# Optimization experiments

Measured on AMD Instinct MI355X. Metric: run time of the kernel, lower is better.

The kernel has to match this reference:

```python
import jax, jax.numpy as jnp
import numpy as np

N = 10000       # nodes
E = 160000      # edges (avg degree 16)
F_IN = 5        # node feature dim
ED = 2          # edge feature dim


def _tconv(x, src, dst, ea, Wq, bq, Wk, bk, Wv, bv, We, Ws, bs, heads, C, concat):
    """PyG TransformerConv (eval mode, root_weight=True, beta=False)."""
    n = x.shape[0]
    q = (x @ Wq + bq).reshape(n, heads, C)
    k = (x @ Wk + bk).reshape(n, heads, C)
    v = (x @ Wv + bv).reshape(n, heads, C)
    e = (ea @ We).reshape(ea.shape[0], heads, C)          # edge embedding, added to key and value
    kj = k[src] + e                                        # [E,H,C] gather source keys
    vj = v[src] + e                                        # [E,H,C] gather source values
    logits = jnp.einsum('ehc,ehc->eh', q[dst], kj) / jnp.sqrt(jnp.asarray(C, x.dtype))
    m = jax.ops.segment_max(logits, dst, num_segments=n)   # stable segment softmax over in-edges
    p = jnp.exp(logits - m[dst])
    s = jax.ops.segment_sum(p, dst, num_segments=n)
    alpha = p / s[dst]                                     # [E,H]
    out = jax.ops.segment_sum(alpha[..., None] * vj, dst, num_segments=n)  # [N,H,C]
    out = out.reshape(n, heads * C) if concat else jnp.mean(out, axis=1)
    return out + x @ Ws + bs                               # root/skip connection


def setup_inputs() -> dict:
    key = jax.random.key(0)
    keys = iter(jax.random.split(key, 64))
    def p(shape):
        return jax.random.normal(next(keys), shape, jnp.float32) * 0.05
    inp = {}
    inp['x'] = jax.random.normal(next(keys), (N, F_IN), jnp.float32)
    inp['edge_src'] = jax.random.randint(next(keys), (E,), 0, N)
    inp['edge_dst'] = jax.random.randint(next(keys), (E,), 0, N)
    inp['edge_attr'] = jax.random.normal(next(keys), (E, ED), jnp.float32)
    # (in_dim, heads, out_channels, concat) for the 3 TransformerConv layers
    layers = [(F_IN, 4, 128, True), (512, 4, 128, True), (512, 1, 64, False)]
    for i, (fin, h, c, concat) in enumerate(layers, 1):
        hc = h * c
        sk = hc if concat else c
        inp[f'Wq{i}'] = p((fin, hc)); inp[f'bq{i}'] = p((hc,))
        inp[f'Wk{i}'] = p((fin, hc)); inp[f'bk{i}'] = p((hc,))
        inp[f'Wv{i}'] = p((fin, hc)); inp[f'bv{i}'] = p((hc,))
        inp[f'We{i}'] = p((ED, hc))   # lin_edge has no bias in PyG
        inp[f'Ws{i}'] = p((fin, sk)); inp[f'bs{i}'] = p((sk,))
    return inp


def reference(x, edge_src, edge_dst, edge_attr,
              Wq1, bq1, Wk1, bk1, Wv1, bv1, We1, Ws1, bs1,
              Wq2, bq2, Wk2, bk2, Wv2, bv2, We2, Ws2, bs2,
              Wq3, bq3, Wk3, bk3, Wv3, bv3, We3, Ws3, bs3):
    h = jax.nn.relu(_tconv(x, edge_src, edge_dst, edge_attr,
                           Wq1, bq1, Wk1, bk1, Wv1, bv1, We1, Ws1, bs1, 4, 128, True))
    h = jax.nn.relu(_tconv(h, edge_src, edge_dst, edge_attr,
                           Wq2, bq2, Wk2, bk2, Wv2, bv2, We2, Ws2, bs2, 4, 128, True))
    return _tconv(h, edge_src, edge_dst, edge_attr,
                  Wq3, bq3, Wk3, bk3, Wv3, bv3, We3, Ws3, bs3, 1, 64, False)
```

## Files before the change

kernel.cpp:

```cpp
#include <hip/hip_runtime.h>

typedef unsigned short u16;
typedef __attribute__((ext_vector_type(8))) short bf16x8;
typedef __attribute__((ext_vector_type(4))) float f32x4;

__device__ __forceinline__ float bf2f(u16 s) {
    return __uint_as_float(((unsigned)s) << 16);
}
__device__ __forceinline__ u16 f2bf(float f) {
    unsigned u = __float_as_uint(f);
    u += 0x7fff + ((u >> 16) & 1);
    return (u16)(u >> 16);
}
__device__ __forceinline__ void unpack8(bf16x8 x, float* f) {
#pragma unroll
    for (int j = 0; j < 8; ++j) f[j] = bf2f((u16)x[j]);
}

__device__ __forceinline__ void gload16(const u16* g, u16* l) {
    __builtin_amdgcn_global_load_lds(
        (const __attribute__((address_space(1))) unsigned*)g,
        (__attribute__((address_space(3))) unsigned*)l, 16, 0, 0);
}

__device__ __forceinline__ float dot8(bf16x8 a, bf16x8 b, float c) {
#if __has_builtin(__builtin_amdgcn_fdot2_f32_bf16)
    typedef __attribute__((ext_vector_type(2))) __bf16 bf16x2;
    union U { bf16x8 v; bf16x2 p[4]; };
    U ua, ub; ua.v = a; ub.v = b;
#pragma unroll
    for (int i = 0; i < 4; ++i)
        c = __builtin_amdgcn_fdot2_f32_bf16(ua.p[i], ub.p[i], c, false);
    return c;
#else
    float fa[8], fb[8];
    unpack8(a, fa); unpack8(b, fb);
#pragma unroll
    for (int j = 0; j < 8; ++j) c = fmaf(fa[j], fb[j], c);
    return c;
#endif
}

struct Ptr8 { const float* p[8]; };
struct PrepArgs { const float* w[8]; const float* b[8]; };

__global__ __launch_bounds__(256)
void prep_weights(PrepArgs a, u16* __restrict__ Wt2, u16* __restrict__ Wt3,
                  float* __restrict__ b2, float* __restrict__ b3) {
    int z = blockIdx.z;
    if (z == 8) {
        if (blockIdx.y != 0 || blockIdx.x >= 9) return;
        int j = blockIdx.x * 256 + threadIdx.x;
        if (j < 2048) b2[j] = a.b[j >> 9][j & 511];
        else if (j < 2304) { int jj = j - 2048; b3[jj] = a.b[4 + (jj >> 6)][jj & 63]; }
        return;
    }
    const float* in;
    u16* out;
    int Nw;
    if (z < 4) { in = a.w[z]; out = Wt2 + (size_t)z * 512 * 512; Nw = 512; }
    else {
        if (blockIdx.y >= 2) return;
        in = a.w[z]; out = Wt3 + (size_t)(z - 4) * 64 * 512; Nw = 64;
    }
    __shared__ float t[32][33];
    int kb = blockIdx.x * 32, nb = blockIdx.y * 32;
    int tx = threadIdx.x & 31, ty = threadIdx.x >> 5;
#pragma unroll
    for (int r = ty; r < 32; r += 8)
        if (nb + tx < Nw)
            t[r][tx] = in[(size_t)(kb + r) * Nw + nb + tx];
    __syncthreads();
#pragma unroll
    for (int r = ty; r < 32; r += 8)
        if (nb + r < Nw)
            out[(size_t)(nb + r) * 512 + kb + tx] = f2bf(t[tx][r]);
}

__global__ __launch_bounds__(256)
void gemm_l1(const float* __restrict__ X, Ptr8 wb, u16* __restrict__ OUT, int N) {
    int wsel = threadIdx.x >> 6;
    int jj = (threadIdx.x & 63) * 8;
    const float* W = wb.p[wsel];
    const float* b = wb.p[4 + wsel];
    float w[5][8], bs[8];
#pragma unroll
    for (int i = 0; i < 5; ++i)
#pragma unroll
        for (int j = 0; j < 8; ++j) w[i][j] = W[(size_t)i * 512 + jj + j];
#pragma unroll
    for (int j = 0; j < 8; ++j) bs[j] = b[jj + j];
    int n0 = blockIdx.x * 8;
    int nend = (N - n0 < 8) ? (N - n0) : 8;
    for (int i = 0; i < nend; ++i) {
        int n = n0 + i;
        float xr[5];
#pragma unroll
        for (int k = 0; k < 5; ++k) xr[k] = X[(size_t)n * 5 + k];
        float acc[8];
#pragma unroll
        for (int j = 0; j < 8; ++j) acc[j] = bs[j];
#pragma unroll
        for (int k = 0; k < 5; ++k)
#pragma unroll
            for (int j = 0; j < 8; ++j) acc[j] = fmaf(xr[k], w[k][j], acc[j]);
        bf16x8 o;
#pragma unroll
        for (int j = 0; j < 8; ++j) o[j] = (short)f2bf(acc[j]);
        *(bf16x8*)(OUT + (size_t)n * 2048 + wsel * 512 + jj) = o;
    }
}

template <int TN>
__global__ __launch_bounds__(256)
void gemm_bf16(const u16* __restrict__ A, const u16* __restrict__ Bt,
               const float* __restrict__ bias, u16* __restrict__ C,
               int M, int Ncols, int K) {
    constexpr int TM = 128, BK = 64;
    constexpr int MFR = (TN == 128) ? 4 : 2;
    constexpr int NFR = 4;
    constexpr int ACH = TM * BK / (256 * 8);
    constexpr int BCH = TN * BK / (256 * 8);

    __shared__ u16 As[TM * BK];
    __shared__ u16 Bs[TN * BK];

    int tid = threadIdx.x;
    int lane = tid & 63;
    int w = tid >> 6;
    int rowbase = blockIdx.x * TM;
    int colbase = blockIdx.y * TN;
    int mwave = (TN == 128) ? (w >> 1) * 64 : w * 32;
    int nwave = (TN == 128) ? (w & 1) * 64 : 0;

    f32x4 acc[MFR][NFR] = {};

    int arow[ACH], asl[ACH];
#pragma unroll
    for (int c = 0; c < ACH; ++c) {
        int idx = c * 256 + tid;
        arow[c] = idx >> 3;
        asl[c] = (idx & 7) ^ (arow[c] & 7);
    }

    for (int k0 = 0; k0 < K; k0 += BK) {
#pragma unroll
        for (int c = 0; c < ACH; ++c) {
            int idx = c * 256 + tid;
            int gr = rowbase + arow[c]; if (gr > M - 1) gr = M - 1;
            gload16(A + (size_t)gr * K + k0 + asl[c] * 8, &As[idx * 8]);
        }
#pragma unroll
        for (int c = 0; c < BCH; ++c) {
            int idx = c * 256 + tid;
            int row = idx >> 3, sl = (idx & 7) ^ (row & 7);
            gload16(Bt + (size_t)(colbase + row) * K + k0 + sl * 8, &Bs[idx * 8]);
        }
        __syncthreads();
#pragma unroll
        for (int kh = 0; kh < 2; ++kh) {
            bf16x8 af[MFR], bfr[NFR];
            int ks = (lane >> 4) + kh * 4;
#pragma unroll
            for (int mi = 0; mi < MFR; ++mi) {
                int r = mwave + mi * 16 + (lane & 15);
                af[mi] = *(const bf16x8*)&As[r * BK + ((ks ^ (r & 7)) * 8)];
            }
#pragma unroll
            for (int ni = 0; ni < NFR; ++ni) {
                int r = nwave + ni * 16 + (lane & 15);
                bfr[ni] = *(const bf16x8*)&Bs[r * BK + ((ks ^ (r & 7)) * 8)];
            }
#pragma unroll
            for (int mi = 0; mi < MFR; ++mi)
#pragma unroll
                for (int ni = 0; ni < NFR; ++ni)
                    acc[mi][ni] = __builtin_amdgcn_mfma_f32_16x16x32_bf16(
                        af[mi], bfr[ni], acc[mi][ni], 0, 0, 0);
        }
        __syncthreads();
    }
#pragma unroll
    for (int mi = 0; mi < MFR; ++mi) {
        int r0 = rowbase + mwave + mi * 16 + (lane >> 4) * 4;
#pragma unroll
        for (int ni = 0; ni < NFR; ++ni) {
            int col = colbase + nwave + ni * 16 + (lane & 15);
            float bv = bias[col];
#pragma unroll
            for (int r = 0; r < 4; ++r) {
                int row = r0 + r;
                if (row < M)
                    C[(size_t)row * Ncols + col] = f2bf(acc[mi][ni][r] + bv);
            }
        }
    }
}

__global__ __launch_bounds__(256)
void histo_dst(const int* __restrict__ dst, int* __restrict__ deg, int E) {
    int i = blockIdx.x * 256 + threadIdx.x;
    if (i < E) atomicAdd(&deg[dst[i]], 1);
}

__global__ __launch_bounds__(1024)
void scan_deg(const int* __restrict__ deg, int* __restrict__ off,
              int* __restrict__ cur, int N) {
    __shared__ int part[1024];
    int t = threadIdx.x;
    int per = (N + 1023) / 1024;
    int base = t * per;
    int s = 0;
    for (int i = 0; i < per; ++i)
        if (base + i < N) s += deg[base + i];
    part[t] = s;
    __syncthreads();
    for (int d = 1; d < 1024; d <<= 1) {
        int v = (t >= d) ? part[t - d] : 0;
        __syncthreads();
        part[t] += v;
        __syncthreads();
    }
    int excl = (t > 0) ? part[t - 1] : 0;
    for (int i = 0; i < per; ++i) {
        int n = base + i;
        if (n < N) {
            off[n] = excl;
            cur[n] = excl;
            excl += deg[n];
        }
    }
    if (t == 1023) off[N] = part[1023];
}

__global__ __launch_bounds__(256)
void scatter_edges(const int* __restrict__ src, const int* __restrict__ dst,
                   const float* __restrict__ EA, int* __restrict__ cur,
                   int* __restrict__ csrc, float2* __restrict__ caxy, int E) {
    int i = blockIdx.x * 256 + threadIdx.x;
    if (i < E) {
        int p = atomicAdd(&cur[dst[i]], 1);
        csrc[p] = src[i];
        caxy[p] = *(const float2*)(EA + 2 * (size_t)i);
    }
}

template <bool RELU>
__global__ __launch_bounds__(256)
void node_attn4(const u16* __restrict__ QKVS, const int* __restrict__ csrc,
                const float2* __restrict__ caxy, const float* __restrict__ We,
                const int* __restrict__ off, u16* __restrict__ OUT,
                int N, float scale) {
    constexpr int SR = 2048, koff = 512, voff = 1024, skoff = 1536;
    constexpr int HC = 512, C = 128, LPG = 16;
    int n = blockIdx.x;
    int w = threadIdx.x >> 6;
    int lane = threadIdx.x & 63;
    int g = lane / LPG;
    int li = lane % LPG;
    int cc = g * C + li * 8;

    const float sc2 = scale * 1.44269504f;
    const u16* nrow = QKVS + (size_t)n * SR;
    bf16x8 q8 = *(const bf16x8*)(nrow + cc);
    float qf[8];
    unpack8(q8, qf);

    float qw0 = 0.f, qw1 = 0.f;
    {
        f32x4 wa = *(const f32x4*)(We + cc), wb = *(const f32x4*)(We + cc + 4);
        f32x4 wc = *(const f32x4*)(We + HC + cc), wd = *(const f32x4*)(We + HC + cc + 4);
#pragma unroll
        for (int j = 0; j < 4; ++j) {
            qw0 = fmaf(qf[j], wa[j], qw0); qw0 = fmaf(qf[4 + j], wb[j], qw0);
            qw1 = fmaf(qf[j], wc[j], qw1); qw1 = fmaf(qf[4 + j], wd[j], qw1);
        }
    }
#pragma unroll
    for (int d = 1; d < LPG; d <<= 1) {
        qw0 += __shfl_xor(qw0, d);
        qw1 += __shfl_xor(qw1, d);
    }
    qw0 *= sc2; qw1 *= sc2;

    int base = off[n];
    int deg = off[n + 1] - base;
    int pdeg = deg < 64 ? deg : 64;
    int ps = 0; float pax = 0.f, pay = 0.f;
    int el = w + 4 * lane;
    if (lane < 16 && el < pdeg) {
        ps = csrc[base + el];
        float2 a = caxy[base + el];
        pax = a.x; pay = a.y;
    }
    int wdeg = (pdeg > w) ? ((pdeg - w + 3) >> 2) : 0;

    float s = 0.f, A0 = 0.f, A1 = 0.f;
    float acc[8] = {};
    const u16* Kp = QKVS + koff;
    const u16* Vp = QKVS + voff;

    auto process = [&](float ax, float ay, bf16x8 k8, bf16x8 v8) {
        float qk = dot8(q8, k8, 0.f);
#pragma unroll
        for (int d = 1; d < LPG; d <<= 1) qk += __shfl_xor(qk, d);
        float lg2 = fmaf(qk, sc2, fmaf(ax, qw0, ay * qw1));
        lg2 = fminf(lg2, 80.f);
        float p = exp2f(lg2);
        s += p;
        A0 = fmaf(p, ax, A0);
        A1 = fmaf(p, ay, A1);
        float vf[8];
        unpack8(v8, vf);
#pragma unroll
        for (int j = 0; j < 8; ++j) acc[j] = fmaf(p, vf[j], acc[j]);
    };

    auto ldp = [&](int t, bf16x8& k8, bf16x8& v8) {
        int tt = t < wdeg ? t : 0;
        int s0 = __shfl(ps, tt);
        k8 = *(const bf16x8*)(Kp + (size_t)s0 * SR + cc);
        v8 = *(const bf16x8*)(Vp + (size_t)s0 * SR + cc);
    };
    if (wdeg > 0) {
        bf16x8 ka0, va0, ka1, va1, kb0, vb0, kb1, vb1;
        ldp(0, ka0, va0); ldp(1, ka1, va1);
        ldp(2, kb0, vb0); ldp(3, kb1, vb1);
        int t = 0;
        for (; t + 2 < wdeg; t += 4) {
            float ax, ay;
            ax = __shfl(pax, t); ay = __shfl(pay, t);
            process(ax, ay, ka0, va0);
            ax = __shfl(pax, t + 1); ay = __shfl(pay, t + 1);
            process(ax, ay, ka1, va1);
            ldp(t + 4, ka0, va0); ldp(t + 5, ka1, va1);
            ax = __shfl(pax, t + 2); ay = __shfl(pay, t + 2);
            process(ax, ay, kb0, vb0);
            if (t + 3 < wdeg) {
                ax = __shfl(pax, t + 3); ay = __shfl(pay, t + 3);
                process(ax, ay, kb1, vb1);
            }
            ldp(t + 6, kb0, vb0); ldp(t + 7, kb1, vb1);
        }
        if (t < wdeg) {
            float ax = __shfl(pax, t), ay = __shfl(pay, t);
            process(ax, ay, ka0, va0);
        }
        if (t + 1 < wdeg) {
            float ax = __shfl(pax, t + 1), ay = __shfl(pay, t + 1);
            process(ax, ay, ka1, va1);
        }
    }
    for (int idx = 64 + w; idx < deg; idx += 4) {
        int s0 = csrc[base + idx];
        float2 a = caxy[base + idx];
        bf16x8 k0 = *(const bf16x8*)(Kp + (size_t)s0 * SR + cc);
        bf16x8 v0 = *(const bf16x8*)(Vp + (size_t)s0 * SR + cc);
        process(a.x, a.y, k0, v0);
    }

    __shared__ float sm[3][64][13];
    if (w > 0) {
        float* d = sm[w - 1][lane];
        d[0] = s; d[1] = A0; d[2] = A1;
#pragma unroll
        for (int j = 0; j < 8; ++j) d[3 + j] = acc[j];
    }
    __syncthreads();
    if (w == 0) {
#pragma unroll
        for (int wv = 0; wv < 3; ++wv) {
            const float* d = sm[wv][lane];
            s += d[0]; A0 += d[1]; A1 += d[2];
#pragma unroll
            for (int j = 0; j < 8; ++j) acc[j] += d[3 + j];
        }
        float inv = (s > 0.f) ? 1.f / s : 0.f;
        float sk[8];
        unpack8(*(const bf16x8*)(nrow + skoff + cc), sk);
        f32x4 wa = *(const f32x4*)(We + cc), wb = *(const f32x4*)(We + cc + 4);
        f32x4 wc = *(const f32x4*)(We + HC + cc), wd = *(const f32x4*)(We + HC + cc + 4);
        float w0[8] = {wa[0], wa[1], wa[2], wa[3], wb[0], wb[1], wb[2], wb[3]};
        float w1[8] = {wc[0], wc[1], wc[2], wc[3], wd[0], wd[1], wd[2], wd[3]};
        bf16x8 ov;
#pragma unroll
        for (int j = 0; j < 8; ++j) {
            float agg = (acc[j] + A0 * w0[j] + A1 * w1[j]) * inv;
            float o = agg + sk[j];
            if (RELU) o = fmaxf(o, 0.f);
            ov[j] = (short)f2bf(o);
        }
        *(bf16x8*)(OUT + (size_t)n * 512 + cc) = ov;
    }
}

template <int H, int C, int LPG, bool RELU>
__global__ __launch_bounds__(256)
void node_attn(const u16* __restrict__ QKVS, int SR, int koff, int voff,
               int skoff, const int* __restrict__ csrc,
               const float2* __restrict__ caxy, const float* __restrict__ We,
               const int* __restrict__ off, float* __restrict__ OUT,
               int OST, int N, float scale) {
    constexpr int HC = H * C;
    constexpr int NG = 64 / LPG;
    int n = blockIdx.x * 4 + (threadIdx.x >> 6);
    if (n >= N) return;
    int lane = threadIdx.x & 63;
    int g = lane / LPG;
    int li = lane % LPG;
    int cc = li * 8;

    const float sc2 = scale * 1.44269504f;
    const u16* nrow = QKVS + (size_t)n * SR;
    bf16x8 q8 = *(const bf16x8*)(nrow + cc);
    float qf[8];
    unpack8(q8, qf);

    float qw0 = 0.f, qw1 = 0.f;
    {
        f32x4 wa = *(const f32x4*)(We + cc), wb = *(const f32x4*)(We + cc + 4);
        f32x4 wc = *(const f32x4*)(We + HC + cc), wd = *(const f32x4*)(We + HC + cc + 4);
#pragma unroll
        for (int j = 0; j < 4; ++j) {
            qw0 = fmaf(qf[j], wa[j], qw0); qw0 = fmaf(qf[4 + j], wb[j], qw0);
            qw1 = fmaf(qf[j], wc[j], qw1); qw1 = fmaf(qf[4 + j], wd[j], qw1);
        }
    }
#pragma unroll
    for (int d = 1; d < LPG; d <<= 1) {
        qw0 += __shfl_xor(qw0, d);
        qw1 += __shfl_xor(qw1, d);
    }
    qw0 *= sc2; qw1 *= sc2;

    int base = off[n];
    int deg = off[n + 1] - base;
    int pdeg = deg < 64 ? deg : 64;
    int ps = 0; float pax = 0.f, pay = 0.f;
    if (lane < pdeg) {
        ps = csrc[base + lane];
        float2 a = caxy[base + lane];
        pax = a.x; pay = a.y;
    }

    float s = 0.f, A0 = 0.f, A1 = 0.f;
    float acc[8] = {};
    const u16* Kp = QKVS + koff;
    const u16* Vp = QKVS + voff;

    auto process = [&](float ax, float ay, bf16x8 k8, bf16x8 v8) {
        float qk = dot8(q8, k8, 0.f);
#pragma unroll
        for (int d = 1; d < LPG; d <<= 1) qk += __shfl_xor(qk, d);
        float lg2 = fmaf(qk, sc2, fmaf(ax, qw0, ay * qw1));
        lg2 = fminf(lg2, 80.f);
        float p = exp2f(lg2);
        s += p;
        A0 = fmaf(p, ax, A0);
        A1 = fmaf(p, ay, A1);
        float vf[8];
        unpack8(v8, vf);
#pragma unroll
        for (int j = 0; j < 8; ++j) acc[j] = fmaf(p, vf[j], acc[j]);
    };

    int trips = (pdeg + NG - 1) / NG;
    for (int k = 0; k < trips; ++k) {
        int idx = g + NG * k;
        bool valid = idx < pdeg;
        int sidx = valid ? idx : (pdeg - 1);
        int s0 = __shfl(ps, sidx);
        float ax0 = __shfl(pax, sidx), ay0 = __shfl(pay, sidx);
        bf16x8 k0 = *(const bf16x8*)(Kp + (size_t)s0 * SR + cc);
        bf16x8 v0 = *(const bf16x8*)(Vp + (size_t)s0 * SR + cc);
        if (valid) process(ax0, ay0, k0, v0);
    }
    int otr = (deg > 64) ? (deg - 64 + NG - 1) / NG : 0;
    for (int k = 0; k < otr; ++k) {
        int idx = 64 + NG * k + g;
        bool valid = idx < deg;
        int ii = valid ? idx : (deg - 1);
        int s0 = csrc[base + ii];
        float2 a = caxy[base + ii];
        bf16x8 k0 = *(const bf16x8*)(Kp + (size_t)s0 * SR + cc);
        bf16x8 v0 = *(const bf16x8*)(Vp + (size_t)s0 * SR + cc);
        if (valid) process(a.x, a.y, k0, v0);
    }
#pragma unroll
    for (int d = LPG; d < 64; d <<= 1) {
        s += __shfl_xor(s, d);
        A0 += __shfl_xor(A0, d);
        A1 += __shfl_xor(A1, d);
#pragma unroll
        for (int j = 0; j < 8; ++j) acc[j] += __shfl_xor(acc[j], d);
    }

    if (g == 0) {
        float inv = (s > 0.f) ? 1.f / s : 0.f;
        float sk[8];
        unpack8(*(const bf16x8*)(nrow + skoff + cc), sk);
        f32x4 wa = *(const f32x4*)(We + cc), wb = *(const f32x4*)(We + cc + 4);
        f32x4 wc = *(const f32x4*)(We + HC + cc), wd = *(const f32x4*)(We + HC + cc + 4);
        float w0[8] = {wa[0], wa[1], wa[2], wa[3], wb[0], wb[1], wb[2], wb[3]};
        float w1[8] = {wc[0], wc[1], wc[2], wc[3], wd[0], wd[1], wd[2], wd[3]};
        float o[8];
#pragma unroll
        for (int j = 0; j < 8; ++j) {
            float agg = (acc[j] + A0 * w0[j] + A1 * w1[j]) * inv;
            o[j] = agg + sk[j];
            if (RELU) o[j] = fmaxf(o[j], 0.f);
        }
        f32x4 oa = {o[0], o[1], o[2], o[3]}, ob = {o[4], o[5], o[6], o[7]};
        *(f32x4*)(OUT + (size_t)n * OST + cc) = oa;
        *(f32x4*)(OUT + (size_t)n * OST + cc + 4) = ob;
    }
}

extern "C" void kernel_launch(void* const* d_in, const int* in_sizes, int n_in,
                              void* d_out, int out_size, void* d_ws, size_t ws_size,
                              hipStream_t stream) {
    const float* x  = (const float*)d_in[0];
    const int* esrc = (const int*)d_in[1];
    const int* edst = (const int*)d_in[2];
    const float* ea = (const float*)d_in[3];
    const int N = in_sizes[0] / 5;
    const int E = in_sizes[1];
    auto in = [&](int i) { return (const float*)d_in[i]; };

    char* p = (char*)d_ws;
    auto alloc = [&](size_t b) {
        char* r = p; p += (b + 255) & ~(size_t)255; return (void*)r;
    };
    u16* QKVS  = (u16*)alloc((size_t)N * 2048 * 2);
    u16* HB    = (u16*)alloc((size_t)N * 512 * 2);
    u16* Wt2   = (u16*)alloc((size_t)2048 * 512 * 2);
    u16* Wt3   = (u16*)alloc((size_t)256 * 512 * 2);
    float* b2  = (float*)alloc(2048 * 4);
    float* b3  = (float*)alloc(256 * 4);
    int* deg   = (int*)alloc((size_t)N * 4);
    int* off   = (int*)alloc((size_t)(N + 1) * 4);
    int* cur   = (int*)alloc((size_t)N * 4);
    int* csrc  = (int*)alloc((size_t)E * 4);
    float2* caxy = (float2*)alloc((size_t)E * 8);

    dim3 b256(256);
    int gE256 = (E + 255) / 256;
    int gM = (N + 127) / 128;
    const float scale128 = 0.08838834764831845f;
    const float scale64  = 0.125f;

    hipMemsetAsync(deg, 0, (size_t)N * sizeof(int), stream);
    histo_dst<<<gE256, b256, 0, stream>>>(edst, deg, E);
    scan_deg<<<1, 1024, 0, stream>>>(deg, off, cur, N);
    scatter_edges<<<gE256, b256, 0, stream>>>(esrc, edst, ea, cur, csrc, caxy, E);

    PrepArgs pa = {{in(13), in(15), in(17), in(20), in(22), in(24), in(26), in(29)},
                   {in(14), in(16), in(18), in(21), in(23), in(25), in(27), in(30)}};
    prep_weights<<<dim3(16, 16, 9), b256, 0, stream>>>(pa, Wt2, Wt3, b2, b3);

    Ptr8 l1 = {{in(4), in(6), in(8), in(11), in(5), in(7), in(9), in(12)}};
    gemm_l1<<<dim3((N + 7) / 8), b256, 0, stream>>>(x, l1, QKVS, N);
    node_attn4<true><<<dim3(N), b256, 0, stream>>>(
        QKVS, csrc, caxy, in(10), off, HB, N, scale128);

    gemm_bf16<128><<<dim3(gM, 16), b256, 0, stream>>>(HB, Wt2, b2, QKVS, N, 2048, 512);
    node_attn4<true><<<dim3(N), b256, 0, stream>>>(
        QKVS, csrc, caxy, in(19), off, HB, N, scale128);

    gemm_bf16<64><<<dim3(gM, 4), b256, 0, stream>>>(HB, Wt3, b3, QKVS, N, 256, 512);
    node_attn<1, 64, 8, false><<<dim3((N + 3) / 4), b256, 0, stream>>>(
        QKVS, 256, 64, 128, 192, csrc, caxy, in(28), off,
        (float*)d_out, 64, N, scale64);
}
```

Baseline: 216.4 us.

## Split attention work by head across blocks, edges across lane groups per wave

The 4-head attention kernel moves from one block per node, with four waves splitting edges and an LDS reduction, to a grid over (head, node group). Each wave now handles one node and one head, and its four 16-lane groups each take a different edge. Partial sums are combined with cross-lane shuffles, so the shared memory and __syncthreads are gone. The old 4-deep software-pipelined K/V prefetch is dropped in favour of a simple loop, which may expose more gather latency. Each head's blocks re-read the node's q, skip and edge-list entries.

```diff
diff --git a/kernel.cpp b/kernel.cpp
--- a/kernel.cpp
+++ b/kernel.cpp
@@ -247,18 +247,19 @@
 
 template <bool RELU>
 __global__ __launch_bounds__(256)
-void node_attn4(const u16* __restrict__ QKVS, const int* __restrict__ csrc,
-                const float2* __restrict__ caxy, const float* __restrict__ We,
-                const int* __restrict__ off, u16* __restrict__ OUT,
-                int N, float scale) {
+void node_attn_h(const u16* __restrict__ QKVS, const int* __restrict__ csrc,
+                 const float2* __restrict__ caxy, const float* __restrict__ We,
+                 const int* __restrict__ off, u16* __restrict__ OUT,
+                 int N, float scale) {
     constexpr int SR = 2048, koff = 512, voff = 1024, skoff = 1536;
-    constexpr int HC = 512, C = 128, LPG = 16;
-    int n = blockIdx.x;
-    int w = threadIdx.x >> 6;
+    constexpr int HC = 512, C = 128, LPG = 16, NG = 4;
+    int h = blockIdx.x;
+    int n = blockIdx.y * 4 + (threadIdx.x >> 6);
+    if (n >= N) return;
     int lane = threadIdx.x & 63;
-    int g = lane / LPG;
-    int li = lane % LPG;
-    int cc = g * C + li * 8;
+    int g = lane >> 4;
+    int li = lane & 15;
+    int cc = h * C + li * 8;
 
     const float sc2 = scale * 1.44269504f;
     const u16* nrow = QKVS + (size_t)n * SR;
@@ -287,13 +288,11 @@
     int deg = off[n + 1] - base;
     int pdeg = deg < 64 ? deg : 64;
     int ps = 0; float pax = 0.f, pay = 0.f;
-    int el = w + 4 * lane;
-    if (lane < 16 && el < pdeg) {
-        ps = csrc[base + el];
-        float2 a = caxy[base + el];
+    if (lane < pdeg) {
+        ps = csrc[base + lane];
+        float2 a = caxy[base + lane];
         pax = a.x; pay = a.y;
     }
-    int wdeg = (pdeg > w) ? ((pdeg - w + 3) >> 2) : 0;
 
     float s = 0.f, A0 = 0.f, A1 = 0.f;
     float acc[8] = {};
@@ -316,65 +315,38 @@
         for (int j = 0; j < 8; ++j) acc[j] = fmaf(p, vf[j], acc[j]);
     };
 
-    auto ldp = [&](int t, bf16x8& k8, bf16x8& v8) {
-        int tt = t < wdeg ? t : 0;
-        int s0 = __shfl(ps, tt);
-        k8 = *(const bf16x8*)(Kp + (size_t)s0 * SR + cc);
-        v8 = *(const bf16x8*)(Vp + (size_t)s0 * SR + cc);
-    };
-    if (wdeg > 0) {
-        bf16x8 ka0, va0, ka1, va1, kb0, vb0, kb1, vb1;
-        ldp(0, ka0, va0); ldp(1, ka1, va1);
-        ldp(2, kb0, vb0); ldp(3, kb1, vb1);
-        int t = 0;
-        for (; t + 2 < wdeg; t += 4) {
-            float ax, ay;
-            ax = __shfl(pax, t); ay = __shfl(pay, t);
-            process(ax, ay, ka0, va0);
-            ax = __shfl(pax, t + 1); ay = __shfl(pay, t + 1);
-            process(ax, ay, ka1, va1);
-            ldp(t + 4, ka0, va0); ldp(t + 5, ka1, va1);
-            ax = __shfl(pax, t + 2); ay = __shfl(pay, t + 2);
-            process(ax, ay, kb0, vb0);
-            if (t + 3 < wdeg) {
-                ax = __shfl(pax, t + 3); ay = __shfl(pay, t + 3);
-                process(ax, ay, kb1, vb1);
-            }
-            ldp(t + 6, kb0, vb0); ldp(t + 7, kb1, vb1);
-        }
-        if (t < wdeg) {
-            float ax = __shfl(pax, t), ay = __shfl(pay, t);
-            process(ax, ay, ka0, va0);
-        }
-        if (t + 1 < wdeg) {
-            float ax = __shfl(pax, t + 1), ay = __shfl(pay, t + 1);
-            process(ax, ay, ka1, va1);
-        }
-    }
-    for (int idx = 64 + w; idx < deg; idx += 4) {
-        int s0 = csrc[base + idx];
-        float2 a = caxy[base + idx];
+    int trips = (pdeg + NG - 1) / NG;
+    for (int k = 0; k < trips; ++k) {
+        int idx = g + NG * k;
+        bool valid = idx < pdeg;
+        int sidx = valid ? idx : (pdeg - 1);
+        int s0 = __shfl(ps, sidx);
+        float ax0 = __shfl(pax, sidx), ay0 = __shfl(pay, sidx);
         bf16x8 k0 = *(const bf16x8*)(Kp + (size_t)s0 * SR + cc);
         bf16x8 v0 = *(const bf16x8*)(Vp + (size_t)s0 * SR + cc);
-        process(a.x, a.y, k0, v0);
-    }
-
-    __shared__ float sm[3][64][13];
-    if (w > 0) {
-        float* d = sm[w - 1][lane];
-        d[0] = s; d[1] = A0; d[2] = A1;
-#pragma unroll
-        for (int j = 0; j < 8; ++j) d[3 + j] = acc[j];
-    }
-    __syncthreads();
-    if (w == 0) {
-#pragma unroll
-        for (int wv = 0; wv < 3; ++wv) {
-            const float* d = sm[wv][lane];
-            s += d[0]; A0 += d[1]; A1 += d[2];
-#pragma unroll
-            for (int j = 0; j < 8; ++j) acc[j] += d[3 + j];
-        }
+        if (valid) process(ax0, ay0, k0, v0);
+    }
+    int otr = (deg > 64) ? (deg - 64 + NG - 1) / NG : 0;
+    for (int k = 0; k < otr; ++k) {
+        int idx = 64 + NG * k + g;
+        bool valid = idx < deg;
+        int ii = valid ? idx : (deg - 1);
+        int s0 = csrc[base + ii];
+        float2 a = caxy[base + ii];
+        bf16x8 k0 = *(const bf16x8*)(Kp + (size_t)s0 * SR + cc);
+        bf16x8 v0 = *(const bf16x8*)(Vp + (size_t)s0 * SR + cc);
+        if (valid) process(a.x, a.y, k0, v0);
+    }
+#pragma unroll
+    for (int d = LPG; d < 64; d <<= 1) {
+        s += __shfl_xor(s, d);
+        A0 += __shfl_xor(A0, d);
+        A1 += __shfl_xor(A1, d);
+#pragma unroll
+        for (int j = 0; j < 8; ++j) acc[j] += __shfl_xor(acc[j], d);
+    }
+
+    if (g == 0) {
         float inv = (s > 0.f) ? 1.f / s : 0.f;
         float sk[8];
         unpack8(*(const bf16x8*)(nrow + skoff + cc), sk);
@@ -546,6 +518,7 @@
     dim3 b256(256);
     int gE256 = (E + 255) / 256;
     int gM = (N + 127) / 128;
+    int gA = (N + 3) / 4;
     const float scale128 = 0.08838834764831845f;
     const float scale64  = 0.125f;
 
@@ -560,15 +533,15 @@
 
     Ptr8 l1 = {{in(4), in(6), in(8), in(11), in(5), in(7), in(9), in(12)}};
     gemm_l1<<<dim3((N + 7) / 8), b256, 0, stream>>>(x, l1, QKVS, N);
-    node_attn4<true><<<dim3(N), b256, 0, stream>>>(
+    node_attn_h<true><<<dim3(4, gA), b256, 0, stream>>>(
         QKVS, csrc, caxy, in(10), off, HB, N, scale128);
 
     gemm_bf16<128><<<dim3(gM, 16), b256, 0, stream>>>(HB, Wt2, b2, QKVS, N, 2048, 512);
-    node_attn4<true><<<dim3(N), b256, 0, stream>>>(
+    node_attn_h<true><<<dim3(4, gA), b256, 0, stream>>>(
         QKVS, csrc, caxy, in(19), off, HB, N, scale128);
 
     gemm_bf16<64><<<dim3(gM, 4), b256, 0, stream>>>(HB, Wt3, b3, QKVS, N, 256, 512);
-    node_attn<1, 64, 8, false><<<dim3((N + 3) / 4), b256, 0, stream>>>(
+    node_attn<1, 64, 8, false><<<dim3(gA), b256, 0, stream>>>(
         QKVS, 256, 64, 128, 192, csrc, caxy, in(28), off,
         (float*)d_out, 64, N, scale64);
 }
```

New measurement: 210.2 us. -2.9%, faster.
